# Optimization experiments

Hardware: AMD Instinct MI355X
Metric: run time of the kernel (lower is better)

The kernel has to match this reference:

```python
import jax, jax.numpy as jnp
import numpy as np

N, E = 32768, 524288
NIN = NOUT = 64
EIN = 32
H, C = 4, 64
HC = H * C


def seg_softmax(logits, seg, num):
    m = jax.ops.segment_max(logits, seg, num_segments=num)
    m = jnp.where(jnp.isfinite(m), m, 0.0)
    ex = jnp.exp(logits - m[seg])
    s = jax.ops.segment_sum(ex, seg, num_segments=num)
    return ex / (s[seg] + 1e-16)


def setup_inputs() -> dict:
    key = jax.random.key(0)
    ks = iter(jax.random.split(key, 48))
    rn = lambda shape, s=0.05: jax.random.normal(next(ks), shape, jnp.float32) * s
    z = lambda shape: jnp.zeros(shape, jnp.float32)
    d = dict(
        x=rn((N, NIN), 1.0),
        edge_attr=rn((E, EIN), 1.0),
        # GINEConv 1: nn = mlp1 (64 -> 64 -> 64), edge lin (32 -> 64), eps
        eps1=z(()), w1a=rn((NIN, 64)), b1a=z((64,)), w1b=rn((64, NOUT)), b1b=z((NOUT,)),
        we1=rn((EIN, NIN)), be1=z((NIN,)),
        # GINEConv 2: nn = mlp2 (64 -> 32 -> 64), edge lin (32 -> 64), eps
        eps2=z(()), w2a=rn((NOUT, 32)), b2a=z((32,)), w2b=rn((32, NOUT)), b2b=z((NOUT,)),
        we2=rn((EIN, NOUT)), be2=z((NOUT,)),
        # TransformerConv(64, 64, heads=4, edge_dim=32)
        wq=rn((NOUT, HC)), bq=z((HC,)), wk=rn((NOUT, HC)), bk=z((HC,)),
        wv=rn((NOUT, HC)), bv=z((HC,)), we3=rn((EIN, HC)),
        wskip=rn((NOUT, HC)), bskip=z((HC,)),
        # GATv2Conv(256, 64, heads=1, edge_dim=32)
        wl=rn((HC, NOUT)), bl=z((NOUT,)), wr=rn((HC, NOUT)), br=z((NOUT,)),
        we4=rn((EIN, NOUT)), att=rn((NOUT,)), bias4=z((NOUT,)),
    )
    d['edge_index'] = jax.random.randint(next(ks), (2, E), 0, N, dtype=jnp.int64)
    return d


def _forward(x, edge_attr, eps1, w1a, b1a, w1b, b1b, we1, be1,
             eps2, w2a, b2a, w2b, b2b, we2, be2,
             wq, bq, wk, bk, wv, bv, we3, wskip, bskip,
             wl, bl, wr, br, we4, att, bias4, edge_index):
    src, dst = edge_index[0], edge_index[1]
    n = x.shape[0]

    # --- GINEConv 1: nn((1+eps)*x + sum_j relu(x_j + lin_e(e_ij))) ---
    e1 = edge_attr @ we1 + be1                                  # (E, NIN)
    agg = jax.ops.segment_sum(jax.nn.relu(x[src] + e1), dst, num_segments=n)
    h = (1.0 + eps1) * x + agg
    x = jax.nn.relu(h @ w1a + b1a) @ w1b + b1b                  # (N, NOUT)

    # --- GINEConv 2 ---
    e2 = edge_attr @ we2 + be2
    agg = jax.ops.segment_sum(jax.nn.relu(x[src] + e2), dst, num_segments=n)
    h = (1.0 + eps2) * x + agg
    x = jax.nn.relu(h @ w2a + b2a) @ w2b + b2b                  # (N, NOUT)

    # --- TransformerConv (heads=4, concat, root skip) ---
    q = (x @ wq + bq).reshape(n, H, C)
    k = (x @ wk + bk).reshape(n, H, C)
    v = (x @ wv + bv).reshape(n, H, C)
    e3 = (edge_attr @ we3).reshape(-1, H, C)
    kj = k[src] + e3
    alpha = jnp.einsum('ehc,ehc->eh', q[dst], kj) / jnp.sqrt(jnp.float32(C))
    alpha = seg_softmax(alpha, dst, n)                          # (E, H)
    msg = (v[src] + e3) * alpha[:, :, None]                     # (E, H, C)
    out = jax.ops.segment_sum(msg, dst, num_segments=n).reshape(n, HC)
    x = out + x @ wskip + bskip                                 # (N, 256)

    # --- GATv2Conv (heads=1) ---
    xl = x @ wl + bl                                            # (N, NOUT)
    xr = x @ wr + br
    e4 = edge_attr @ we4
    hmsg = jax.nn.leaky_relu(xl[src] + xr[dst] + e4, 0.2)       # (E, NOUT)
    logit = hmsg @ att                                          # (E,)
    a = seg_softmax(logit, dst, n)
    x = jax.ops.segment_sum(xl[src] * a[:, None], dst, num_segments=n) + bias4
    return x


def reference(x, edge_attr, eps1, w1a, b1a, w1b, b1b, we1, be1,
              eps2, w2a, b2a, w2b, b2b, we2, be2,
              wq, bq, wk, bk, wv, bv, we3, wskip, bskip,
              wl, bl, wr, br, we4, att, bias4, edge_index):
    return _forward(x, edge_attr, eps1, w1a, b1a, w1b, b1b, we1, be1,
                    eps2, w2a, b2a, w2b, b2b, we2, be2,
                    wq, bq, wk, bk, wv, bv, we3, wskip, bskip,
                    wl, bl, wr, br, we4, att, bias4, edge_index)
```

## Files before the change

kernel.cpp:

```cpp
#include <hip/hip_runtime.h>
#include <math.h>


typedef __attribute__((ext_vector_type(2))) _Float16 half2v;
typedef __attribute__((ext_vector_type(4))) _Float16 half4v;
typedef __attribute__((ext_vector_type(8))) _Float16 half8v;
typedef __attribute__((ext_vector_type(4))) float float4v;

__global__ void k_detect(const unsigned int* __restrict__ w, int* __restrict__ flag)
{
    __shared__ int any;
    if (threadIdx.x == 0) any = 0;
    __syncthreads();
    int found = 0;
    for (int i = threadIdx.x; i < 2048; i += 256)
        if (w[2 * i + 1] != 0u) found = 1;
    if (found) atomicOr(&any, 1);
    __syncthreads();
    if (threadIdx.x == 0) flag[0] = any ? 0 : 1;
}

__global__ void k_cvt(const void* __restrict__ eidx, const int* __restrict__ flag,
                      int* __restrict__ out, int* __restrict__ counts, int E)
{
    int i = blockIdx.x * blockDim.x + threadIdx.x;
    if (i >= 2 * E) return;
    int v = flag[0] ? (int)((const long long*)eidx)[i] : ((const int*)eidx)[i];
    out[i] = v;
    if (i >= E) atomicAdd(&counts[v], 1);
}

__global__ void k_scan(const int* __restrict__ counts, int* __restrict__ offs,
                       int* __restrict__ cursor, int N)
{
    __shared__ int part[1024];
    int t = threadIdx.x;
    int base = t * 32;
    int loc[32];
    int s = 0;
#pragma unroll
    for (int i = 0; i < 32; i++) { loc[i] = counts[base + i]; s += loc[i]; }
    part[t] = s;
    __syncthreads();
    for (int off = 1; off < 1024; off <<= 1) {
        int v = (t >= off) ? part[t - off] : 0;
        __syncthreads();
        part[t] += v;
        __syncthreads();
    }
    int run = part[t] - s;
#pragma unroll
    for (int i = 0; i < 32; i++) {
        offs[base + i] = run;
        cursor[base + i] = run;
        run += loc[i];
    }
    if (t == 1023) offs[N] = run;
}

__global__ void k_scatter(const int* __restrict__ dst, const int* __restrict__ srcA,
                          int* __restrict__ cursor, int* __restrict__ perm,
                          int* __restrict__ sperm, int* __restrict__ pos, int E)
{
    int i = blockIdx.x * blockDim.x + threadIdx.x;
    if (i < E) {
        int d = dst[i];
        int p = atomicAdd(&cursor[d], 1);
        perm[p] = i;
        sperm[p] = srcA[i];
        pos[i] = p;
    }
}

__global__ __launch_bounds__(256) void k_eap(const float* __restrict__ ea,
                                             const int* __restrict__ pos,
                                             _Float16* __restrict__ eap)
{
    int t = threadIdx.x;
    int i = blockIdx.x * 64 + (t >> 2);
    int ks = (t & 3) * 8;
    float4 a0 = *(const float4*)&ea[(size_t)i * 32 + ks];
    float4 a1 = *(const float4*)&ea[(size_t)i * 32 + ks + 4];
    half8v h8;
    h8[0] = (_Float16)a0.x; h8[1] = (_Float16)a0.y;
    h8[2] = (_Float16)a0.z; h8[3] = (_Float16)a0.w;
    h8[4] = (_Float16)a1.x; h8[5] = (_Float16)a1.y;
    h8[6] = (_Float16)a1.z; h8[7] = (_Float16)a1.w;
    int p = pos[i];
    *(half8v*)&eap[(size_t)p * 32 + ks] = h8;
}

__global__ __launch_bounds__(256) void k_emm(
    const _Float16* __restrict__ eap,
    const _Float16* __restrict__ WtA, const float* __restrict__ beA,
    _Float16* __restrict__ epA,
    const _Float16* __restrict__ WtB, const float* __restrict__ beB,
    _Float16* __restrict__ epB, int dual)
{
    int t = threadIdx.x;
    int wid = t >> 6, l = t & 63;
    int jb = (blockIdx.x * 4 + wid) * 16;
    int cr = l & 15, kg = l >> 4;
    half8v a = *(const half8v*)&eap[(size_t)(jb + cr) * 32 + kg * 8];
    int orow = kg * 4;
#pragma unroll
    for (int c = 0; c < 4; c++) {
        half8v b = *(const half8v*)&WtA[(size_t)(c * 16 + cr) * 32 + kg * 8];
        float4v d = __builtin_amdgcn_mfma_f32_16x16x32_f16(a, b, (float4v){0.f,0.f,0.f,0.f}, 0, 0, 0);
        int col = c * 16 + cr;
        float bv = beA ? beA[col] : 0.f;
#pragma unroll
        for (int r = 0; r < 4; r++)
            epA[(size_t)(jb + orow + r) * 64 + col] = (_Float16)(d[r] + bv);
    }
    if (dual) {
#pragma unroll
        for (int c = 0; c < 4; c++) {
            half8v b = *(const half8v*)&WtB[(size_t)(c * 16 + cr) * 32 + kg * 8];
            float4v d = __builtin_amdgcn_mfma_f32_16x16x32_f16(a, b, (float4v){0.f,0.f,0.f,0.f}, 0, 0, 0);
            int col = c * 16 + cr;
            float bv = beB ? beB[col] : 0.f;
#pragma unroll
            for (int r = 0; r < 4; r++)
                epB[(size_t)(jb + orow + r) * 64 + col] = (_Float16)(d[r] + bv);
        }
    }
}

__global__ __launch_bounds__(256) void k_egv(
    const float* __restrict__ ea, const int* __restrict__ perm,
    const float* __restrict__ weA, const float* __restrict__ beA,
    _Float16* __restrict__ epA,
    const float* __restrict__ weB, const float* __restrict__ beB,
    _Float16* __restrict__ epB, int dual)
{
    int t = threadIdx.x;
    int wid = t >> 6, lane = t & 63;
    float wA[32];
#pragma unroll
    for (int k = 0; k < 32; k++) wA[k] = weA[k * 64 + lane];
    float bAc = beA ? beA[lane] : 0.f;
    float wB[32];
    float bBc = 0.f;
    if (dual) {
#pragma unroll
        for (int k = 0; k < 32; k++) wB[k] = weB[k * 64 + lane];
        bBc = beB ? beB[lane] : 0.f;
    }
    int jbase = (blockIdx.x * 4 + wid) * 8;
    for (int u = 0; u < 8; u++) {
        int j = jbase + u;
        int e = __builtin_amdgcn_readfirstlane(perm[j]);
        const float4* ea4 = (const float4*)(ea + (size_t)e * 32);
        float eav[32];
#pragma unroll
        for (int w = 0; w < 8; w++) {
            float4 t4 = ea4[w];
            eav[4 * w] = t4.x; eav[4 * w + 1] = t4.y;
            eav[4 * w + 2] = t4.z; eav[4 * w + 3] = t4.w;
        }
        float vA = bAc;
#pragma unroll
        for (int k = 0; k < 32; k++) vA = fmaf(eav[k], wA[k], vA);
        epA[(size_t)j * 64 + lane] = (_Float16)vA;
        if (dual) {
            float vB = bBc;
#pragma unroll
            for (int k = 0; k < 32; k++) vB = fmaf(eav[k], wB[k], vB);
            epB[(size_t)j * 64 + lane] = (_Float16)vB;
        }
    }
}

__global__ __launch_bounds__(256) void k_prep(
    const float* __restrict__ x, int NX,
    const float* __restrict__ wq, const float* __restrict__ wk,
    const float* __restrict__ wv, const float* __restrict__ wskip,
    const float* __restrict__ wl, const float* __restrict__ wr,
    const float* __restrict__ w1a, const float* __restrict__ w1b,
    const float* __restrict__ w2a, const float* __restrict__ w2b,
    const float* __restrict__ we3, const float* __restrict__ bq,
    const float* __restrict__ we1, const float* __restrict__ we2,
    const float* __restrict__ we4,
    _Float16* __restrict__ xh,
    _Float16* __restrict__ Wtq, _Float16* __restrict__ Wtk,
    _Float16* __restrict__ Wtv, _Float16* __restrict__ Wts,
    _Float16* __restrict__ Wtl, _Float16* __restrict__ Wtr,
    _Float16* __restrict__ Wt1a, _Float16* __restrict__ Wt1b,
    _Float16* __restrict__ Wt2a, _Float16* __restrict__ Wt2b,
    _Float16* __restrict__ Mt, float* __restrict__ cst,
    _Float16* __restrict__ we3r,
    _Float16* __restrict__ Wt1e, _Float16* __restrict__ Wt2e,
    _Float16* __restrict__ Wt4e)
{
    int g = blockIdx.x * 256 + threadIdx.x;
    if (g < 16384) {
        int c = g >> 6, k = g & 63;
        Wtq[g] = (_Float16)wq[(size_t)k * 256 + c];
        Wtk[g] = (_Float16)wk[(size_t)k * 256 + c];
        Wtv[g] = (_Float16)wv[(size_t)k * 256 + c];
        Wts[g] = (_Float16)wskip[(size_t)k * 256 + c];
    } else if (g < 32768) {
        int q = g - 16384, c = q >> 8, k = q & 255;
        Wtl[q] = (_Float16)wl[(size_t)k * 64 + c];
        Wtr[q] = (_Float16)wr[(size_t)k * 64 + c];
    } else if (g < 36864) {
        int q = g - 32768, m = q >> 6, k = q & 63;
        Wt1a[q] = (_Float16)w1a[(size_t)k * 64 + m];
        Wt1b[q] = (_Float16)w1b[(size_t)k * 64 + m];
    } else if (g < 38912) {
        int q = g - 36864, m = q >> 6, k = q & 63;
        Wt2a[q] = (_Float16)w2a[(size_t)k * 32 + m];
    } else if (g < 40960) {
        int q = g - 38912, c = q >> 5, k = q & 31;
        Wt2b[q] = (_Float16)w2b[(size_t)k * 64 + c];
    } else if (g < 49152) {
        int q = g - 40960, m = q >> 6, d = q & 63;
        int h = m >> 5, kk = m & 31;
        float s = 0.f;
        for (int c = 0; c < 64; c++)
            s = fmaf(wq[(size_t)d * 256 + h * 64 + c],
                     we3[(size_t)kk * 256 + h * 64 + c], s);
        Mt[q] = (_Float16)(0.125f * s);
    } else if (g < 49280) {
        int m = g - 49152, h = m >> 5, kk = m & 31;
        float s = 0.f;
        for (int c = 0; c < 64; c++)
            s = fmaf(bq[h * 64 + c], we3[(size_t)kk * 256 + h * 64 + c], s);
        cst[m] = 0.125f * s;
    } else if (g < 57472) {
        int q = g - 49280;
        int kk = q >> 10, ph = (q >> 9) & 1, lane = (q >> 3) & 63, i = q & 7;
        int slot = lane >> 4, hh = (lane >> 2) & 3, ss = lane & 3;
        we3r[q] = (_Float16)we3[(size_t)(slot * 8 + kk) * 256
                                + hh * 64 + ss * 16 + ph * 8 + i];
    } else if (g < 59520) {
        int q = g - 57472, c = q >> 5, k = q & 31;
        Wt1e[q] = (_Float16)we1[(size_t)k * 64 + c];
    } else if (g < 61568) {
        int q = g - 59520, c = q >> 5, k = q & 31;
        Wt2e[q] = (_Float16)we2[(size_t)k * 64 + c];
    } else if (g < 63616) {
        int q = g - 61568, c = q >> 5, k = q & 31;
        Wt4e[q] = (_Float16)we4[(size_t)k * 64 + c];
    }
    for (int i = g; i < NX; i += 256 * 256)
        xh[i] = (_Float16)x[i];
}

template<int MID>
__global__ __launch_bounds__(256) void k_mlp(
    const _Float16* __restrict__ A,
    const _Float16* __restrict__ Wt1, const float* __restrict__ b1,
    const _Float16* __restrict__ Wt2, const float* __restrict__ b2,
    _Float16* __restrict__ out)
{
    __shared__ _Float16 As[64][72];
    __shared__ _Float16 Ws1[MID][72];
    __shared__ _Float16 Ws2[64][MID + 8];
    __shared__ _Float16 mids[64][MID + 8];
    int t = threadIdx.x;
    int n0 = blockIdx.x * 64;
    for (int f = t; f < 512; f += 256) {
        int r = f >> 3, seg = f & 7;
        *(uint4*)&As[r][seg * 8] = *(const uint4*)&A[(size_t)(n0 + r) * 64 + seg * 8];
    }
    for (int f = t; f < MID * 8; f += 256) {
        int r = f >> 3, seg = f & 7;
        *(uint4*)&Ws1[r][seg * 8] = *(const uint4*)&Wt1[(size_t)r * 64 + seg * 8];
    }
    constexpr int CH = MID / 8;
    for (int f = t; f < 64 * CH; f += 256) {
        int r = f / CH, seg = f % CH;
        *(uint4*)&Ws2[r][seg * 8] = *(const uint4*)&Wt2[(size_t)r * MID + seg * 8];
    }
    __syncthreads();
    int w = t >> 6, l = t & 63;
    int arow = w * 16 + (l & 15);
    int kg = (l >> 4) * 8;
    int colg = l & 15;
    int orow = w * 16 + (l >> 4) * 4;
    half8v a0 = *(const half8v*)&As[arow][kg];
    half8v a1 = *(const half8v*)&As[arow][32 + kg];
    constexpr int NCT1 = MID / 16;
#pragma unroll
    for (int ct = 0; ct < NCT1; ct++) {
        half8v b0 = *(const half8v*)&Ws1[ct * 16 + colg][kg];
        half8v b1v = *(const half8v*)&Ws1[ct * 16 + colg][32 + kg];
        float4v acc = {0.f, 0.f, 0.f, 0.f};
        acc = __builtin_amdgcn_mfma_f32_16x16x32_f16(a0, b0, acc, 0, 0, 0);
        acc = __builtin_amdgcn_mfma_f32_16x16x32_f16(a1, b1v, acc, 0, 0, 0);
        int col = ct * 16 + colg;
        float bb = b1[col];
#pragma unroll
        for (int r = 0; r < 4; r++)
            mids[orow + r][col] = (_Float16)fmaxf(acc[r] + bb, 0.f);
    }
    __syncthreads();
    half8v m0 = *(const half8v*)&mids[arow][kg];
#pragma unroll
    for (int ct = 0; ct < 4; ct++) {
        half8v b0 = *(const half8v*)&Ws2[ct * 16 + colg][kg];
        float4v acc = {0.f, 0.f, 0.f, 0.f};
        acc = __builtin_amdgcn_mfma_f32_16x16x32_f16(m0, b0, acc, 0, 0, 0);
        if (MID == 64) {
            half8v m1 = *(const half8v*)&mids[arow][32 + kg];
            half8v b1v = *(const half8v*)&Ws2[ct * 16 + colg][32 + kg];
            acc = __builtin_amdgcn_mfma_f32_16x16x32_f16(m1, b1v, acc, 0, 0, 0);
        }
        int col = ct * 16 + colg;
        float bb = b2[col];
#pragma unroll
        for (int r = 0; r < 4; r++)
            out[(size_t)(n0 + orow + r) * 64 + col] = (_Float16)(acc[r] + bb);
    }
}

__global__ __launch_bounds__(256) void k_gemm4m(
    const _Float16* __restrict__ A,
    const _Float16* __restrict__ Wtq, const float* __restrict__ bq,
    const _Float16* __restrict__ Wtk, const float* __restrict__ bk,
    const _Float16* __restrict__ Wtv, const float* __restrict__ bv,
    const _Float16* __restrict__ Wts, const float* __restrict__ bs,
    const _Float16* __restrict__ Mt,  const float* __restrict__ cst,
    _Float16* __restrict__ qbh, _Float16* __restrict__ kbh,
    _Float16* __restrict__ vbh, float* __restrict__ skipb,
    _Float16* __restrict__ qtp)
{
    __shared__ _Float16 As[64][72];
    __shared__ _Float16 Ws[128][72];
    int t = threadIdx.x;
    int n0 = blockIdx.x * 64;
    int y = blockIdx.y;
    for (int f = t; f < 512; f += 256) {
        int r = f >> 3, seg = f & 7;
        *(uint4*)&As[r][seg * 8] = *(const uint4*)&A[(size_t)(n0 + r) * 64 + seg * 8];
    }
    if (y < 16) {
        int p = y >> 2, j0 = (y & 3) * 64;
        const _Float16* Wt = (p == 0) ? Wtq : (p == 1) ? Wtk : (p == 2) ? Wtv : Wts;
        for (int f = t; f < 512; f += 256) {
            int c = f >> 3, seg = f & 7;
            *(uint4*)&Ws[c][seg * 8] = *(const uint4*)&Wt[(size_t)(j0 + c) * 64 + seg * 8];
        }
    } else {
        for (int f = t; f < 1024; f += 256) {
            int c = f >> 3, seg = f & 7;
            *(uint4*)&Ws[c][seg * 8] = *(const uint4*)&Mt[(size_t)c * 64 + seg * 8];
        }
    }
    __syncthreads();
    int w = t >> 6, l = t & 63;
    int arow = w * 16 + (l & 15);
    int kg = (l >> 4) * 8;
    int colg = l & 15;
    int orow = w * 16 + (l >> 4) * 4;
    half8v a0 = *(const half8v*)&As[arow][kg];
    half8v a1 = *(const half8v*)&As[arow][32 + kg];
    if (y < 16) {
        int p = y >> 2, j0 = (y & 3) * 64;
        const float* B = (p == 0) ? bq : (p == 1) ? bk : (p == 2) ? bv : bs;
        float4v acc[4];
#pragma unroll
        for (int ct = 0; ct < 4; ct++) {
            half8v b0 = *(const half8v*)&Ws[ct * 16 + colg][kg];
            half8v b1 = *(const half8v*)&Ws[ct * 16 + colg][32 + kg];
            float4v a = {0.f, 0.f, 0.f, 0.f};
            a = __builtin_amdgcn_mfma_f32_16x16x32_f16(a0, b0, a, 0, 0, 0);
            a = __builtin_amdgcn_mfma_f32_16x16x32_f16(a1, b1, a, 0, 0, 0);
            acc[ct] = a;
        }
#pragma unroll
        for (int ct = 0; ct < 4; ct++) {
            int col = j0 + ct * 16 + colg;
            float bb = B[col];
            if (p == 3) {
#pragma unroll
                for (int r = 0; r < 4; r++)
                    skipb[(size_t)(n0 + orow + r) * 256 + col] = acc[ct][r] + bb;
            } else {
                _Float16* O = (p == 0) ? qbh : (p == 1) ? kbh : vbh;
#pragma unroll
                for (int r = 0; r < 4; r++)
                    O[(size_t)(n0 + orow + r) * 256 + col] = (_Float16)(acc[ct][r] + bb);
            }
        }
    } else {
        float4v acc[8];
#pragma unroll
        for (int ct = 0; ct < 8; ct++) {
            half8v b0 = *(const half8v*)&Ws[ct * 16 + colg][kg];
            half8v b1 = *(const half8v*)&Ws[ct * 16 + colg][32 + kg];
            float4v a = {0.f, 0.f, 0.f, 0.f};
            a = __builtin_amdgcn_mfma_f32_16x16x32_f16(a0, b0, a, 0, 0, 0);
            a = __builtin_amdgcn_mfma_f32_16x16x32_f16(a1, b1, a, 0, 0, 0);
            acc[ct] = a;
        }
#pragma unroll
        for (int ct = 0; ct < 8; ct++) {
            int col = ct * 16 + colg;
            float bb = cst[col];
#pragma unroll
            for (int r = 0; r < 4; r++)
                qtp[(size_t)(n0 + orow + r) * 128 + col] = (_Float16)(acc[ct][r] + bb);
        }
    }
}

__global__ __launch_bounds__(256) void k_gatgemm(
    const float* __restrict__ A,
    const _Float16* __restrict__ WtL, const float* __restrict__ bL,
    const _Float16* __restrict__ WtR, const float* __restrict__ bR,
    _Float16* __restrict__ xlh, _Float16* __restrict__ xrh)
{
    __shared__ _Float16 As[64][136];
    __shared__ _Float16 Ws[64][136];
    int t = threadIdx.x;
    int n0 = blockIdx.x * 64;
    int y = blockIdx.y;
    const _Float16* Wt = y ? WtR : WtL;
    const float* bb = y ? bR : bL;
    _Float16* out = y ? xrh : xlh;
    int w = t >> 6, l = t & 63;
    int arow = w * 16 + (l & 15);
    int kg = (l >> 4) * 8;
    int colg = l & 15;
    int orow = w * 16 + (l >> 4) * 4;
    float4v acc[4] = {{0.f,0.f,0.f,0.f},{0.f,0.f,0.f,0.f},
                      {0.f,0.f,0.f,0.f},{0.f,0.f,0.f,0.f}};
    for (int kh = 0; kh < 2; kh++) {
        __syncthreads();
        for (int f = t; f < 2048; f += 256) {
            int r = f >> 5, seg = f & 31;
            float4 v = *(const float4*)&A[(size_t)(n0 + r) * 256 + kh * 128 + seg * 4];
            half4v hv;
            hv[0] = (_Float16)v.x; hv[1] = (_Float16)v.y;
            hv[2] = (_Float16)v.z; hv[3] = (_Float16)v.w;
            *(half4v*)&As[r][seg * 4] = hv;
        }
        for (int f = t; f < 1024; f += 256) {
            int c = f >> 4, seg = f & 15;
            *(uint4*)&Ws[c][seg * 8] = *(const uint4*)&Wt[(size_t)c * 256 + kh * 128 + seg * 8];
        }
        __syncthreads();
#pragma unroll
        for (int ks = 0; ks < 4; ks++) {
            half8v a = *(const half8v*)&As[arow][ks * 32 + kg];
#pragma unroll
            for (int ct = 0; ct < 4; ct++) {
                half8v b = *(const half8v*)&Ws[ct * 16 + colg][ks * 32 + kg];
                acc[ct] = __builtin_amdgcn_mfma_f32_16x16x32_f16(a, b, acc[ct], 0, 0, 0);
            }
        }
    }
#pragma unroll
    for (int ct = 0; ct < 4; ct++) {
        int col = ct * 16 + colg;
        float bv = bb[col];
#pragma unroll
        for (int r = 0; r < 4; r++)
            out[(size_t)(n0 + orow + r) * 64 + col] = (_Float16)(acc[ct][r] + bv);
    }
}

__global__ __launch_bounds__(256) void k_gine2(
    const _Float16* __restrict__ xin, const _Float16* __restrict__ ep,
    const float* __restrict__ epsp,
    const int* __restrict__ offs, const int* __restrict__ sperm,
    _Float16* __restrict__ hout)
{
    int t = threadIdx.x;
    int wid  = __builtin_amdgcn_readfirstlane(t >> 6);
    int n    = blockIdx.x * 4 + wid;
    int lane = t & 63;
    int g = lane >> 4, li = lane & 15, c0 = li * 4;
    int j0 = __builtin_amdgcn_readfirstlane(offs[n]);
    int j1 = __builtin_amdgcn_readfirstlane(offs[n + 1]);
    float4 acc = {0.f, 0.f, 0.f, 0.f};
    for (int jq = j0; jq < j1; jq += 4) {
        int j = jq + g;
        int jc = (j < j1) ? j : (j1 - 1);
        int s = sperm[jc];
        half4v ev = *(const half4v*)&ep[(size_t)jc * 64 + c0];
        half4v xv = *(const half4v*)&xin[(size_t)s * 64 + c0];
        if (j < j1) {
            acc.x += fmaxf((float)xv[0] + (float)ev[0], 0.f);
            acc.y += fmaxf((float)xv[1] + (float)ev[1], 0.f);
            acc.z += fmaxf((float)xv[2] + (float)ev[2], 0.f);
            acc.w += fmaxf((float)xv[3] + (float)ev[3], 0.f);
        }
    }
    acc.x += __shfl_xor(acc.x, 16); acc.x += __shfl_xor(acc.x, 32);
    acc.y += __shfl_xor(acc.y, 16); acc.y += __shfl_xor(acc.y, 32);
    acc.z += __shfl_xor(acc.z, 16); acc.z += __shfl_xor(acc.z, 32);
    acc.w += __shfl_xor(acc.w, 16); acc.w += __shfl_xor(acc.w, 32);
    if (g == 0) {
        float eps1 = 1.f + epsp[0];
        half4v xn = *(const half4v*)&xin[(size_t)n * 64 + c0];
        half4v o;
        o[0] = (_Float16)(eps1 * (float)xn[0] + acc.x);
        o[1] = (_Float16)(eps1 * (float)xn[1] + acc.y);
        o[2] = (_Float16)(eps1 * (float)xn[2] + acc.z);
        o[3] = (_Float16)(eps1 * (float)xn[3] + acc.w);
        *(half4v*)&hout[(size_t)n * 64 + c0] = o;
    }
}

template<int USE_EAP>
__global__ __launch_bounds__(256) void k_tconv4(
    const _Float16* __restrict__ qb, const _Float16* __restrict__ kb,
    const _Float16* __restrict__ vb, const _Float16* __restrict__ qtp,
    const _Float16* __restrict__ we3r, const _Float16* __restrict__ eap,
    const float* __restrict__ ea, const int* __restrict__ perm,
    const int* __restrict__ offs, const int* __restrict__ sperm,
    float* __restrict__ skip_io)
{
    __shared__ _Float16 we3s[8192];
    __shared__ float wa_s[4][4][32];
    int t = threadIdx.x;
    ((uint4*)we3s)[t]       = ((const uint4*)we3r)[t];
    ((uint4*)we3s)[t + 256] = ((const uint4*)we3r)[t + 256];
    ((uint4*)we3s)[t + 512] = ((const uint4*)we3r)[t + 512];
    ((uint4*)we3s)[t + 768] = ((const uint4*)we3r)[t + 768];
    int wid = __builtin_amdgcn_readfirstlane(t >> 6);
    int n = blockIdx.x * 4 + wid;
    int lane = t & 63;
    int g = lane >> 4, li = lane & 15;
    int h = li >> 2, sub = li & 3;
    int ch0 = h * 64 + sub * 16;
    float qs[16];
    {
        half8v q0 = *(const half8v*)&qb[(size_t)n * 256 + ch0];
        half8v q1 = *(const half8v*)&qb[(size_t)n * 256 + ch0 + 8];
#pragma unroll
        for (int i = 0; i < 8; i++) {
            qs[i] = (float)q0[i] * 0.125f;
            qs[8 + i] = (float)q1[i] * 0.125f;
        }
    }
    float qtf[8];
    {
        half8v qt8 = *(const half8v*)&qtp[(size_t)n * 128 + h * 32 + sub * 8];
#pragma unroll
        for (int i = 0; i < 8; i++) qtf[i] = (float)qt8[i];
    }
    int j0 = __builtin_amdgcn_readfirstlane(offs[n]);
    int j1 = __builtin_amdgcn_readfirstlane(offs[n + 1]);
    float l = 0.f;
    float acc[16] = {};
    float wa[8] = {};
    for (int jq = j0; jq < j1; jq += 4) {
        int j = jq + g;
        int jc = (j < j1) ? j : (j1 - 1);
        int s = sperm[jc];
        const _Float16* kr = &kb[(size_t)s * 256 + ch0];
        half8v k0 = *(const half8v*)kr;
        half8v k1 = *(const half8v*)(kr + 8);
        float ef[8];
        if (USE_EAP) {
            half8v e8 = *(const half8v*)&eap[(size_t)jc * 32 + sub * 8];
#pragma unroll
            for (int i = 0; i < 8; i++) ef[i] = (float)e8[i];
        } else {
            int e = perm[jc];
            float4 a0 = *(const float4*)&ea[(size_t)e * 32 + sub * 8];
            float4 a1 = *(const float4*)&ea[(size_t)e * 32 + sub * 8 + 4];
            ef[0] = a0.x; ef[1] = a0.y; ef[2] = a0.z; ef[3] = a0.w;
            ef[4] = a1.x; ef[5] = a1.y; ef[6] = a1.z; ef[7] = a1.w;
        }
        float p = 0.f;
#pragma unroll
        for (int i = 0; i < 8; i++)
            p += qs[i] * (float)k0[i] + qs[8 + i] * (float)k1[i];
#pragma unroll
        for (int i = 0; i < 8; i++) p += qtf[i] * ef[i];
        p += __shfl_xor(p, 1);
        p += __shfl_xor(p, 2);
        float w = (j < j1) ? __expf(p) : 0.f;
        const _Float16* vr = &vb[(size_t)s * 256 + ch0];
        half8v v0 = *(const half8v*)vr;
        half8v v1 = *(const half8v*)(vr + 8);
        l += w;
#pragma unroll
        for (int i = 0; i < 8; i++) {
            acc[i] = fmaf(w, (float)v0[i], acc[i]);
            acc[8 + i] = fmaf(w, (float)v1[i], acc[8 + i]);
        }
#pragma unroll
        for (int i = 0; i < 8; i++) wa[i] = fmaf(w, ef[i], wa[i]);
    }
    l += __shfl_xor(l, 16); l += __shfl_xor(l, 32);
#pragma unroll
    for (int i = 0; i < 16; i++) {
        acc[i] += __shfl_xor(acc[i], 16);
        acc[i] += __shfl_xor(acc[i], 32);
    }
#pragma unroll
    for (int i = 0; i < 8; i++) {
        wa[i] += __shfl_xor(wa[i], 16);
        wa[i] += __shfl_xor(wa[i], 32);
    }
    if (g == 0) {
#pragma unroll
        for (int i = 0; i < 8; i++) wa_s[wid][h][sub * 8 + i] = wa[i];
    }
    __syncthreads();
    float corr[16] = {};
#pragma unroll
    for (int kk = 0; kk < 8; kk++) {
        float wv = wa_s[wid][h][g * 8 + kk];
        half8v w3a = *(const half8v*)&we3s[kk * 1024 + lane * 8];
        half8v w3b = *(const half8v*)&we3s[kk * 1024 + 512 + lane * 8];
#pragma unroll
        for (int i = 0; i < 8; i++) {
            corr[i] = fmaf(wv, (float)w3a[i], corr[i]);
            corr[8 + i] = fmaf(wv, (float)w3b[i], corr[8 + i]);
        }
    }
#pragma unroll
    for (int i = 0; i < 16; i++) {
        corr[i] += __shfl_xor(corr[i], 16);
        corr[i] += __shfl_xor(corr[i], 32);
    }
    if (g == 0) {
        float rl = 1.f / (l + 1e-16f);
        size_t o = (size_t)n * 256 + ch0;
#pragma unroll
        for (int i = 0; i < 16; i += 4) {
            float4 sk = *(const float4*)&skip_io[o + i];
            float4 ov;
            ov.x = (acc[i]     + corr[i])     * rl + sk.x;
            ov.y = (acc[i + 1] + corr[i + 1]) * rl + sk.y;
            ov.z = (acc[i + 2] + corr[i + 2]) * rl + sk.z;
            ov.w = (acc[i + 3] + corr[i + 3]) * rl + sk.w;
            *(float4*)&skip_io[o + i] = ov;
        }
    }
}

__global__ __launch_bounds__(256) void k_gat2(
    const _Float16* __restrict__ xl, const _Float16* __restrict__ xr,
    const _Float16* __restrict__ e4p,
    const float* __restrict__ attv, const float* __restrict__ bias4,
    const int* __restrict__ offs, const int* __restrict__ sperm,
    float* __restrict__ out)
{
    int t = threadIdx.x;
    int wid  = __builtin_amdgcn_readfirstlane(t >> 6);
    int n    = blockIdx.x * 4 + wid;
    int lane = t & 63;
    int g = lane >> 4, li = lane & 15, c0 = li * 4;
    half4v xrh = *(const half4v*)&xr[(size_t)n * 64 + c0];
    float xr0 = (float)xrh[0], xr1 = (float)xrh[1];
    float xr2 = (float)xrh[2], xr3 = (float)xrh[3];
    float4 av  = *(const float4*)&attv[c0];
    int j0 = __builtin_amdgcn_readfirstlane(offs[n]);
    int j1 = __builtin_amdgcn_readfirstlane(offs[n + 1]);
    float l = 0.f;
    float4 acc = {0.f, 0.f, 0.f, 0.f};
    for (int jq = j0; jq < j1; jq += 4) {
        int j = jq + g;
        int jc = (j < j1) ? j : (j1 - 1);
        int s = sperm[jc];
        half4v ev = *(const half4v*)&e4p[(size_t)jc * 64 + c0];
        half4v xlv = *(const half4v*)&xl[(size_t)s * 64 + c0];
        float x0 = (float)xlv[0], x1 = (float)xlv[1];
        float x2 = (float)xlv[2], x3 = (float)xlv[3];
        float h0 = x0 + xr0 + (float)ev[0];
        float h1 = x1 + xr1 + (float)ev[1];
        float h2 = x2 + xr2 + (float)ev[2];
        float h3 = x3 + xr3 + (float)ev[3];
        h0 = (h0 > 0.f) ? h0 : 0.2f * h0;
        h1 = (h1 > 0.f) ? h1 : 0.2f * h1;
        h2 = (h2 > 0.f) ? h2 : 0.2f * h2;
        h3 = (h3 > 0.f) ? h3 : 0.2f * h3;
        float p = h0 * av.x + h1 * av.y + h2 * av.z + h3 * av.w;
        p += __shfl_xor(p, 1); p += __shfl_xor(p, 2);
        p += __shfl_xor(p, 4); p += __shfl_xor(p, 8);
        float w = (j < j1) ? __expf(p) : 0.f;
        l += w;
        acc.x = fmaf(w, x0, acc.x);
        acc.y = fmaf(w, x1, acc.y);
        acc.z = fmaf(w, x2, acc.z);
        acc.w = fmaf(w, x3, acc.w);
    }
    l += __shfl_xor(l, 16); l += __shfl_xor(l, 32);
    acc.x += __shfl_xor(acc.x, 16); acc.x += __shfl_xor(acc.x, 32);
    acc.y += __shfl_xor(acc.y, 16); acc.y += __shfl_xor(acc.y, 32);
    acc.z += __shfl_xor(acc.z, 16); acc.z += __shfl_xor(acc.z, 32);
    acc.w += __shfl_xor(acc.w, 16); acc.w += __shfl_xor(acc.w, 32);
    if (g == 0) {
        float rl = 1.f / (l + 1e-16f);
        float4 bv = *(const float4*)&bias4[c0];
        float4 o;
        o.x = acc.x * rl + bv.x;
        o.y = acc.y * rl + bv.y;
        o.z = acc.z * rl + bv.z;
        o.w = acc.w * rl + bv.w;
        *(float4*)&out[(size_t)n * 64 + c0] = o;
    }
}

extern "C" void kernel_launch(void* const* d_in, const int* in_sizes, int n_in,
                              void* d_out, int out_size, void* d_ws, size_t ws_size,
                              hipStream_t stream)
{
    const float* x     = (const float*)d_in[0];
    const float* ea    = (const float*)d_in[1];
    const float* eps1  = (const float*)d_in[2];
    const float* w1a   = (const float*)d_in[3];
    const float* b1a   = (const float*)d_in[4];
    const float* w1b   = (const float*)d_in[5];
    const float* b1b   = (const float*)d_in[6];
    const float* we1   = (const float*)d_in[7];
    const float* be1   = (const float*)d_in[8];
    const float* eps2  = (const float*)d_in[9];
    const float* w2a   = (const float*)d_in[10];
    const float* b2a   = (const float*)d_in[11];
    const float* w2b   = (const float*)d_in[12];
    const float* b2b   = (const float*)d_in[13];
    const float* we2   = (const float*)d_in[14];
    const float* be2   = (const float*)d_in[15];
    const float* wq    = (const float*)d_in[16];
    const float* bq    = (const float*)d_in[17];
    const float* wk    = (const float*)d_in[18];
    const float* bk    = (const float*)d_in[19];
    const float* wv    = (const float*)d_in[20];
    const float* bv    = (const float*)d_in[21];
    const float* we3   = (const float*)d_in[22];
    const float* wskip = (const float*)d_in[23];
    const float* bskip = (const float*)d_in[24];
    const float* wl    = (const float*)d_in[25];
    const float* bl    = (const float*)d_in[26];
    const float* wr    = (const float*)d_in[27];
    const float* br    = (const float*)d_in[28];
    const float* we4   = (const float*)d_in[29];
    const float* attv  = (const float*)d_in[30];
    const float* bias4 = (const float*)d_in[31];
    const void*  eidx  = d_in[32];

    const int N = in_sizes[0] / 64;
    const int E = in_sizes[1] / 32;

    char* ws = (char*)d_ws;
    size_t off = 0;
    auto alloc = [&](size_t bytes) {
        void* p = ws + off;
        off += (bytes + 255) & ~(size_t)255;
        return p;
    };
    int* flag    = (int*)alloc(4);
    int* econv   = (int*)alloc((size_t)2 * E * 4);
    int* counts  = (int*)alloc((size_t)N * 4);
    int* cursor  = (int*)alloc((size_t)N * 4);
    int* offs    = (int*)alloc((size_t)(N + 1) * 4);
    int* perm    = (int*)alloc((size_t)E * 4);
    int* sperm   = (int*)alloc((size_t)E * 4);
    int* pos     = (int*)alloc((size_t)E * 4);
    _Float16* xh  = (_Float16*)alloc((size_t)N * 64 * 2);
    _Float16* h16 = (_Float16*)alloc((size_t)N * 64 * 2);
    _Float16* x1h = (_Float16*)alloc((size_t)N * 64 * 2);
    _Float16* x2h = (_Float16*)alloc((size_t)N * 64 * 2);
    _Float16* Wtq = (_Float16*)alloc(16384 * 2);
    _Float16* Wtk = (_Float16*)alloc(16384 * 2);
    _Float16* Wtv = (_Float16*)alloc(16384 * 2);
    _Float16* Wts = (_Float16*)alloc(16384 * 2);
    _Float16* Wtl = (_Float16*)alloc(16384 * 2);
    _Float16* Wtr = (_Float16*)alloc(16384 * 2);
    _Float16* Wt1a = (_Float16*)alloc(4096 * 2);
    _Float16* Wt1b = (_Float16*)alloc(4096 * 2);
    _Float16* Wt2a = (_Float16*)alloc(2048 * 2);
    _Float16* Wt2b = (_Float16*)alloc(2048 * 2);
    _Float16* Mt   = (_Float16*)alloc(8192 * 2);
    float*    cst  = (float*)alloc(128 * 4);
    _Float16* we3r = (_Float16*)alloc(8192 * 2);
    _Float16* Wt1e = (_Float16*)alloc(2048 * 2);
    _Float16* Wt2e = (_Float16*)alloc(2048 * 2);
    _Float16* Wt4e = (_Float16*)alloc(2048 * 2);
    char* R = (char*)alloc((size_t)2 * E * 64 * 2);
    _Float16* e1p   = (_Float16*)R;
    _Float16* e2p   = e1p + (size_t)E * 64;
    _Float16* qbh   = (_Float16*)R;
    _Float16* kbh   = qbh + (size_t)N * 256;
    _Float16* vbh   = kbh + (size_t)N * 256;
    float*    skipb = (float*)(R + (size_t)3 * N * 256 * 2);
    _Float16* qtp   = (_Float16*)(R + (size_t)3 * N * 256 * 2 + (size_t)N * 256 * 4);
    _Float16* e4p   = (_Float16*)R;
    _Float16* xlh   = h16;
    _Float16* xrh   = x1h;
    size_t base_off = off;
    _Float16* eap = (_Float16*)alloc((size_t)E * 32 * 2);
    int use_eap = (off <= ws_size) ? 1 : 0;

    if (base_off > ws_size) return;

    k_prep<<<256, 256, 0, stream>>>(x, N * 64, wq, wk, wv, wskip, wl, wr,
                                    w1a, w1b, w2a, w2b, we3, bq, we1, we2, we4,
                                    xh, Wtq, Wtk, Wtv, Wts, Wtl, Wtr,
                                    Wt1a, Wt1b, Wt2a, Wt2b, Mt, cst,
                                    we3r, Wt1e, Wt2e, Wt4e);

    k_detect<<<1, 256, 0, stream>>>((const unsigned int*)eidx, flag);
    hipMemsetAsync(counts, 0, (size_t)N * 4, stream);
    k_cvt<<<(2 * E + 255) / 256, 256, 0, stream>>>(eidx, flag, econv, counts, E);
    const int* srcI = econv;
    const int* dstI = econv + E;

    k_scan<<<1, 1024, 0, stream>>>(counts, offs, cursor, N);
    k_scatter<<<(E + 255) / 256, 256, 0, stream>>>(dstI, srcI, cursor, perm, sperm,
                                                   pos, E);

    if (use_eap) {
        k_eap<<<E / 64, 256, 0, stream>>>(ea, pos, eap);
        k_emm<<<E / 64, 256, 0, stream>>>(eap, Wt1e, be1, e1p, Wt2e, be2, e2p, 1);
    } else {
        k_egv<<<E / 32, 256, 0, stream>>>(ea, perm, we1, be1, e1p, we2, be2, e2p, 1);
    }

    k_gine2<<<N / 4, 256, 0, stream>>>(xh, e1p, eps1, offs, sperm, h16);
    k_mlp<64><<<N / 64, 256, 0, stream>>>(h16, Wt1a, b1a, Wt1b, b1b, x1h);

    k_gine2<<<N / 4, 256, 0, stream>>>(x1h, e2p, eps2, offs, sperm, h16);
    k_mlp<32><<<N / 64, 256, 0, stream>>>(h16, Wt2a, b2a, Wt2b, b2b, x2h);

    k_gemm4m<<<dim3(N / 64, 17), 256, 0, stream>>>(x2h,
                                                   Wtq, bq, Wtk, bk, Wtv, bv,
                                                   Wts, bskip, Mt, cst,
                                                   qbh, kbh, vbh, skipb, qtp);
    if (use_eap)
        k_tconv4<1><<<N / 4, 256, 0, stream>>>(qbh, kbh, vbh, qtp, we3r, eap,
                                               ea, perm, offs, sperm, skipb);
    else
        k_tconv4<0><<<N / 4, 256, 0, stream>>>(qbh, kbh, vbh, qtp, we3r, eap,
                                               ea, perm, offs, sperm, skipb);

    k_gatgemm<<<dim3(N / 64, 2), 256, 0, stream>>>(skipb, Wtl, bl, Wtr, br, xlh, xrh);
    if (use_eap)
        k_emm<<<E / 64, 256, 0, stream>>>(eap, Wt4e, (const float*)nullptr, e4p,
                                          (const _Float16*)nullptr,
                                          (const float*)nullptr,
                                          (_Float16*)nullptr, 0);
    else
        k_egv<<<E / 32, 256, 0, stream>>>(ea, perm, we4, (const float*)nullptr, e4p,
                                          (const float*)nullptr,
                                          (const float*)nullptr,
                                          (_Float16*)nullptr, 0);
    k_gat2<<<N / 4, 256, 0, stream>>>(xlh, xrh, e4p, attv, bias4, offs, sperm,
                                      (float*)d_out);
}
```

Before: 401.4 us.

## Fold Q/K/V projections into 64-dim source features for transformer conv

Rewrites the TransformerConv stage algebraically. Attention logits now come from a precomputed Wq·Wk^T product applied to the destination node, dotted with the raw 64-dim source features. Values are aggregated in input space and projected once per node by a new post kernel, using a concatenated [Wv; We3] matrix. This removes the per-node K/V 256-wide GEMM outputs and shrinks per-edge gather traffic. It also fuses the edge-attr fp16 permutation into the scatter kernel and merges the two GAT linear GEMMs into one launch. The costs are an extra kernel and fp16 intermediate buffers, which may change numerical precision.

```diff
diff --git a/kernel.cpp b/kernel.cpp
--- a/kernel.cpp
+++ b/kernel.cpp
@@ -58,36 +58,32 @@
     if (t == 1023) offs[N] = run;
 }
 
+template<int WEAP>
 __global__ void k_scatter(const int* __restrict__ dst, const int* __restrict__ srcA,
                           int* __restrict__ cursor, int* __restrict__ perm,
-                          int* __restrict__ sperm, int* __restrict__ pos, int E)
+                          int* __restrict__ sperm, const float* __restrict__ ea,
+                          _Float16* __restrict__ eap, int E)
 {
     int i = blockIdx.x * blockDim.x + threadIdx.x;
-    if (i < E) {
-        int d = dst[i];
-        int p = atomicAdd(&cursor[d], 1);
-        perm[p] = i;
-        sperm[p] = srcA[i];
-        pos[i] = p;
-    }
-}
-
-__global__ __launch_bounds__(256) void k_eap(const float* __restrict__ ea,
-                                             const int* __restrict__ pos,
-                                             _Float16* __restrict__ eap)
-{
-    int t = threadIdx.x;
-    int i = blockIdx.x * 64 + (t >> 2);
-    int ks = (t & 3) * 8;
-    float4 a0 = *(const float4*)&ea[(size_t)i * 32 + ks];
-    float4 a1 = *(const float4*)&ea[(size_t)i * 32 + ks + 4];
-    half8v h8;
-    h8[0] = (_Float16)a0.x; h8[1] = (_Float16)a0.y;
-    h8[2] = (_Float16)a0.z; h8[3] = (_Float16)a0.w;
-    h8[4] = (_Float16)a1.x; h8[5] = (_Float16)a1.y;
-    h8[6] = (_Float16)a1.z; h8[7] = (_Float16)a1.w;
-    int p = pos[i];
-    *(half8v*)&eap[(size_t)p * 32 + ks] = h8;
+    if (i >= E) return;
+    int d = dst[i];
+    int p = atomicAdd(&cursor[d], 1);
+    perm[p] = i;
+    sperm[p] = srcA[i];
+    if (WEAP) {
+        const float4* r = (const float4*)(ea + (size_t)i * 32);
+        half8v* o = (half8v*)(eap + (size_t)p * 32);
+#pragma unroll
+        for (int w = 0; w < 4; w++) {
+            float4 a = r[2 * w], b = r[2 * w + 1];
+            half8v h8;
+            h8[0] = (_Float16)a.x; h8[1] = (_Float16)a.y;
+            h8[2] = (_Float16)a.z; h8[3] = (_Float16)a.w;
+            h8[4] = (_Float16)b.x; h8[5] = (_Float16)b.y;
+            h8[6] = (_Float16)b.z; h8[7] = (_Float16)b.w;
+            o[w] = h8;
+        }
+    }
 }
 
 __global__ __launch_bounds__(256) void k_emm(
@@ -183,68 +179,79 @@
     const float* __restrict__ we1, const float* __restrict__ we2,
     const float* __restrict__ we4,
     _Float16* __restrict__ xh,
-    _Float16* __restrict__ Wtq, _Float16* __restrict__ Wtk,
-    _Float16* __restrict__ Wtv, _Float16* __restrict__ Wts,
+    _Float16* __restrict__ Wts, _Float16* __restrict__ Gt,
     _Float16* __restrict__ Wtl, _Float16* __restrict__ Wtr,
     _Float16* __restrict__ Wt1a, _Float16* __restrict__ Wt1b,
     _Float16* __restrict__ Wt2a, _Float16* __restrict__ Wt2b,
     _Float16* __restrict__ Mt, float* __restrict__ cst,
-    _Float16* __restrict__ we3r,
     _Float16* __restrict__ Wt1e, _Float16* __restrict__ Wt2e,
-    _Float16* __restrict__ Wt4e)
+    _Float16* __restrict__ Wt4e, float* __restrict__ zt,
+    _Float16* __restrict__ Bt3)
 {
     int g = blockIdx.x * 256 + threadIdx.x;
     if (g < 16384) {
         int c = g >> 6, k = g & 63;
-        Wtq[g] = (_Float16)wq[(size_t)k * 256 + c];
-        Wtk[g] = (_Float16)wk[(size_t)k * 256 + c];
-        Wtv[g] = (_Float16)wv[(size_t)k * 256 + c];
         Wts[g] = (_Float16)wskip[(size_t)k * 256 + c];
     } else if (g < 32768) {
-        int q = g - 16384, c = q >> 8, k = q & 255;
+        int q = g - 16384, col = q >> 6, d = q & 63;
+        int h = col >> 6, c = col & 63;
+        float s = 0.f;
+        for (int mq = 0; mq < 64; mq++)
+            s = fmaf(wq[(size_t)d * 256 + h * 64 + mq],
+                     wk[(size_t)c * 256 + h * 64 + mq], s);
+        Gt[q] = (_Float16)(0.125f * s);
+    } else if (g < 49152) {
+        int q = g - 32768, c = q >> 8, k = q & 255;
         Wtl[q] = (_Float16)wl[(size_t)k * 64 + c];
         Wtr[q] = (_Float16)wr[(size_t)k * 64 + c];
-    } else if (g < 36864) {
-        int q = g - 32768, m = q >> 6, k = q & 63;
+    } else if (g < 53248) {
+        int q = g - 49152, m = q >> 6, k = q & 63;
         Wt1a[q] = (_Float16)w1a[(size_t)k * 64 + m];
         Wt1b[q] = (_Float16)w1b[(size_t)k * 64 + m];
-    } else if (g < 38912) {
-        int q = g - 36864, m = q >> 6, k = q & 63;
+    } else if (g < 55296) {
+        int q = g - 53248, m = q >> 6, k = q & 63;
         Wt2a[q] = (_Float16)w2a[(size_t)k * 32 + m];
-    } else if (g < 40960) {
-        int q = g - 38912, c = q >> 5, k = q & 31;
+    } else if (g < 57344) {
+        int q = g - 55296, c = q >> 5, k = q & 31;
         Wt2b[q] = (_Float16)w2b[(size_t)k * 64 + c];
-    } else if (g < 49152) {
-        int q = g - 40960, m = q >> 6, d = q & 63;
+    } else if (g < 65536) {
+        int q = g - 57344, m = q >> 6, d = q & 63;
         int h = m >> 5, kk = m & 31;
         float s = 0.f;
         for (int c = 0; c < 64; c++)
             s = fmaf(wq[(size_t)d * 256 + h * 64 + c],
                      we3[(size_t)kk * 256 + h * 64 + c], s);
         Mt[q] = (_Float16)(0.125f * s);
-    } else if (g < 49280) {
-        int m = g - 49152, h = m >> 5, kk = m & 31;
+    } else if (g < 65664) {
+        int m = g - 65536, h = m >> 5, kk = m & 31;
         float s = 0.f;
         for (int c = 0; c < 64; c++)
             s = fmaf(bq[h * 64 + c], we3[(size_t)kk * 256 + h * 64 + c], s);
         cst[m] = 0.125f * s;
-    } else if (g < 57472) {
-        int q = g - 49280;
-        int kk = q >> 10, ph = (q >> 9) & 1, lane = (q >> 3) & 63, i = q & 7;
-        int slot = lane >> 4, hh = (lane >> 2) & 3, ss = lane & 3;
-        we3r[q] = (_Float16)we3[(size_t)(slot * 8 + kk) * 256
-                                + hh * 64 + ss * 16 + ph * 8 + i];
-    } else if (g < 59520) {
-        int q = g - 57472, c = q >> 5, k = q & 31;
+    } else if (g < 67712) {
+        int q = g - 65664, c = q >> 5, k = q & 31;
         Wt1e[q] = (_Float16)we1[(size_t)k * 64 + c];
-    } else if (g < 61568) {
-        int q = g - 59520, c = q >> 5, k = q & 31;
+    } else if (g < 69760) {
+        int q = g - 67712, c = q >> 5, k = q & 31;
         Wt2e[q] = (_Float16)we2[(size_t)k * 64 + c];
-    } else if (g < 63616) {
-        int q = g - 61568, c = q >> 5, k = q & 31;
+    } else if (g < 71808) {
+        int q = g - 69760, c = q >> 5, k = q & 31;
         Wt4e[q] = (_Float16)we4[(size_t)k * 64 + c];
-    }
-    for (int i = g; i < NX; i += 256 * 256)
+    } else if (g < 72064) {
+        int q = g - 71808, h = q >> 6, c = q & 63;
+        float s = 0.f;
+        for (int mq = 0; mq < 64; mq++)
+            s = fmaf(wk[(size_t)c * 256 + h * 64 + mq], bq[h * 64 + mq], s);
+        zt[q] = 0.125f * s;
+    } else if (g < 96640) {
+        int q = g - 72064;
+        int hc = q / 96, k = q - hc * 96;
+        int h = hc >> 6, col = hc & 63;
+        float v = (k < 64) ? wv[(size_t)k * 256 + h * 64 + col]
+                           : we3[(size_t)(k - 64) * 256 + h * 64 + col];
+        Bt3[q] = (_Float16)v;
+    }
+    for (int i = g; i < NX; i += 512 * 256)
         xh[i] = (_Float16)x[i];
 }
 
@@ -318,13 +325,10 @@
 
 __global__ __launch_bounds__(256) void k_gemm4m(
     const _Float16* __restrict__ A,
-    const _Float16* __restrict__ Wtq, const float* __restrict__ bq,
-    const _Float16* __restrict__ Wtk, const float* __restrict__ bk,
-    const _Float16* __restrict__ Wtv, const float* __restrict__ bv,
+    const _Float16* __restrict__ Gt,
     const _Float16* __restrict__ Wts, const float* __restrict__ bs,
     const _Float16* __restrict__ Mt,  const float* __restrict__ cst,
-    _Float16* __restrict__ qbh, _Float16* __restrict__ kbh,
-    _Float16* __restrict__ vbh, float* __restrict__ skipb,
+    _Float16* __restrict__ Yb, _Float16* __restrict__ skiph,
     _Float16* __restrict__ qtp)
 {
     __shared__ _Float16 As[64][72];
@@ -336,9 +340,9 @@
         int r = f >> 3, seg = f & 7;
         *(uint4*)&As[r][seg * 8] = *(const uint4*)&A[(size_t)(n0 + r) * 64 + seg * 8];
     }
-    if (y < 16) {
-        int p = y >> 2, j0 = (y & 3) * 64;
-        const _Float16* Wt = (p == 0) ? Wtq : (p == 1) ? Wtk : (p == 2) ? Wtv : Wts;
+    if (y < 8) {
+        int j0 = (y & 3) * 64;
+        const _Float16* Wt = (y < 4) ? Gt : Wts;
         for (int f = t; f < 512; f += 256) {
             int c = f >> 3, seg = f & 7;
             *(uint4*)&Ws[c][seg * 8] = *(const uint4*)&Wt[(size_t)(j0 + c) * 64 + seg * 8];
@@ -357,10 +361,9 @@
     int orow = w * 16 + (l >> 4) * 4;
     half8v a0 = *(const half8v*)&As[arow][kg];
     half8v a1 = *(const half8v*)&As[arow][32 + kg];
-    if (y < 16) {
-        int p = y >> 2, j0 = (y & 3) * 64;
-        const float* B = (p == 0) ? bq : (p == 1) ? bk : (p == 2) ? bv : bs;
-        float4v acc[4];
+    if (y < 8) {
+        int j0 = (y & 3) * 64;
+        _Float16* O = (y < 4) ? Yb : skiph;
 #pragma unroll
         for (int ct = 0; ct < 4; ct++) {
             half8v b0 = *(const half8v*)&Ws[ct * 16 + colg][kg];
@@ -368,25 +371,13 @@
             float4v a = {0.f, 0.f, 0.f, 0.f};
             a = __builtin_amdgcn_mfma_f32_16x16x32_f16(a0, b0, a, 0, 0, 0);
             a = __builtin_amdgcn_mfma_f32_16x16x32_f16(a1, b1, a, 0, 0, 0);
-            acc[ct] = a;
-        }
-#pragma unroll
-        for (int ct = 0; ct < 4; ct++) {
             int col = j0 + ct * 16 + colg;
-            float bb = B[col];
-            if (p == 3) {
-#pragma unroll
-                for (int r = 0; r < 4; r++)
-                    skipb[(size_t)(n0 + orow + r) * 256 + col] = acc[ct][r] + bb;
-            } else {
-                _Float16* O = (p == 0) ? qbh : (p == 1) ? kbh : vbh;
-#pragma unroll
-                for (int r = 0; r < 4; r++)
-                    O[(size_t)(n0 + orow + r) * 256 + col] = (_Float16)(acc[ct][r] + bb);
-            }
+            float bb = (y < 4) ? 0.f : bs[col];
+#pragma unroll
+            for (int r = 0; r < 4; r++)
+                O[(size_t)(n0 + orow + r) * 256 + col] = (_Float16)(a[r] + bb);
         }
     } else {
-        float4v acc[8];
 #pragma unroll
         for (int ct = 0; ct < 8; ct++) {
             half8v b0 = *(const half8v*)&Ws[ct * 16 + colg][kg];
@@ -394,72 +385,12 @@
             float4v a = {0.f, 0.f, 0.f, 0.f};
             a = __builtin_amdgcn_mfma_f32_16x16x32_f16(a0, b0, a, 0, 0, 0);
             a = __builtin_amdgcn_mfma_f32_16x16x32_f16(a1, b1, a, 0, 0, 0);
-            acc[ct] = a;
-        }
-#pragma unroll
-        for (int ct = 0; ct < 8; ct++) {
             int col = ct * 16 + colg;
             float bb = cst[col];
 #pragma unroll
             for (int r = 0; r < 4; r++)
-                qtp[(size_t)(n0 + orow + r) * 128 + col] = (_Float16)(acc[ct][r] + bb);
-        }
-    }
-}
-
-__global__ __launch_bounds__(256) void k_gatgemm(
-    const float* __restrict__ A,
-    const _Float16* __restrict__ WtL, const float* __restrict__ bL,
-    const _Float16* __restrict__ WtR, const float* __restrict__ bR,
-    _Float16* __restrict__ xlh, _Float16* __restrict__ xrh)
-{
-    __shared__ _Float16 As[64][136];
-    __shared__ _Float16 Ws[64][136];
-    int t = threadIdx.x;
-    int n0 = blockIdx.x * 64;
-    int y = blockIdx.y;
-    const _Float16* Wt = y ? WtR : WtL;
-    const float* bb = y ? bR : bL;
-    _Float16* out = y ? xrh : xlh;
-    int w = t >> 6, l = t & 63;
-    int arow = w * 16 + (l & 15);
-    int kg = (l >> 4) * 8;
-    int colg = l & 15;
-    int orow = w * 16 + (l >> 4) * 4;
-    float4v acc[4] = {{0.f,0.f,0.f,0.f},{0.f,0.f,0.f,0.f},
-                      {0.f,0.f,0.f,0.f},{0.f,0.f,0.f,0.f}};
-    for (int kh = 0; kh < 2; kh++) {
-        __syncthreads();
-        for (int f = t; f < 2048; f += 256) {
-            int r = f >> 5, seg = f & 31;
-            float4 v = *(const float4*)&A[(size_t)(n0 + r) * 256 + kh * 128 + seg * 4];
-            half4v hv;
-            hv[0] = (_Float16)v.x; hv[1] = (_Float16)v.y;
-            hv[2] = (_Float16)v.z; hv[3] = (_Float16)v.w;
-            *(half4v*)&As[r][seg * 4] = hv;
-        }
-        for (int f = t; f < 1024; f += 256) {
-            int c = f >> 4, seg = f & 15;
-            *(uint4*)&Ws[c][seg * 8] = *(const uint4*)&Wt[(size_t)c * 256 + kh * 128 + seg * 8];
-        }
-        __syncthreads();
-#pragma unroll
-        for (int ks = 0; ks < 4; ks++) {
-            half8v a = *(const half8v*)&As[arow][ks * 32 + kg];
-#pragma unroll
-            for (int ct = 0; ct < 4; ct++) {
-                half8v b = *(const half8v*)&Ws[ct * 16 + colg][ks * 32 + kg];
-                acc[ct] = __builtin_amdgcn_mfma_f32_16x16x32_f16(a, b, acc[ct], 0, 0, 0);
-            }
-        }
-    }
-#pragma unroll
-    for (int ct = 0; ct < 4; ct++) {
-        int col = ct * 16 + colg;
-        float bv = bb[col];
-#pragma unroll
-        for (int r = 0; r < 4; r++)
-            out[(size_t)(n0 + orow + r) * 64 + col] = (_Float16)(acc[ct][r] + bv);
+                qtp[(size_t)(n0 + orow + r) * 128 + col] = (_Float16)(a[r] + bb);
+        }
     }
 }
 
@@ -507,133 +438,205 @@
 }
 
 template<int USE_EAP>
-__global__ __launch_bounds__(256) void k_tconv4(
-    const _Float16* __restrict__ qb, const _Float16* __restrict__ kb,
-    const _Float16* __restrict__ vb, const _Float16* __restrict__ qtp,
-    const _Float16* __restrict__ we3r, const _Float16* __restrict__ eap,
-    const float* __restrict__ ea, const int* __restrict__ perm,
-    const int* __restrict__ offs, const int* __restrict__ sperm,
-    float* __restrict__ skip_io)
-{
-    __shared__ _Float16 we3s[8192];
-    __shared__ float wa_s[4][4][32];
-    int t = threadIdx.x;
-    ((uint4*)we3s)[t]       = ((const uint4*)we3r)[t];
-    ((uint4*)we3s)[t + 256] = ((const uint4*)we3r)[t + 256];
-    ((uint4*)we3s)[t + 512] = ((const uint4*)we3r)[t + 512];
-    ((uint4*)we3s)[t + 768] = ((const uint4*)we3r)[t + 768];
+__global__ __launch_bounds__(256) void k_tconv5(
+    const _Float16* __restrict__ Yb, const _Float16* __restrict__ qtp,
+    const float* __restrict__ zt, const _Float16* __restrict__ x2h,
+    const _Float16* __restrict__ eap, const float* __restrict__ ea,
+    const int* __restrict__ perm, const int* __restrict__ offs,
+    const int* __restrict__ sperm,
+    _Float16* __restrict__ xaccb, _Float16* __restrict__ wab,
+    float* __restrict__ lb)
+{
+    int t = threadIdx.x;
     int wid = __builtin_amdgcn_readfirstlane(t >> 6);
     int n = blockIdx.x * 4 + wid;
     int lane = t & 63;
-    int g = lane >> 4, li = lane & 15;
-    int h = li >> 2, sub = li & 3;
-    int ch0 = h * 64 + sub * 16;
-    float qs[16];
+    int h = lane >> 4, c = lane & 15;
+    float yb0, yb1, yb2, yb3;
     {
-        half8v q0 = *(const half8v*)&qb[(size_t)n * 256 + ch0];
-        half8v q1 = *(const half8v*)&qb[(size_t)n * 256 + ch0 + 8];
-#pragma unroll
-        for (int i = 0; i < 8; i++) {
-            qs[i] = (float)q0[i] * 0.125f;
-            qs[8 + i] = (float)q1[i] * 0.125f;
-        }
-    }
-    float qtf[8];
-    {
-        half8v qt8 = *(const half8v*)&qtp[(size_t)n * 128 + h * 32 + sub * 8];
-#pragma unroll
-        for (int i = 0; i < 8; i++) qtf[i] = (float)qt8[i];
-    }
+        half4v Y4 = *(const half4v*)&Yb[(size_t)n * 256 + h * 64 + c * 4];
+        float4 z4 = *(const float4*)&zt[h * 64 + c * 4];
+        yb0 = (float)Y4[0] + z4.x; yb1 = (float)Y4[1] + z4.y;
+        yb2 = (float)Y4[2] + z4.z; yb3 = (float)Y4[3] + z4.w;
+    }
+    half2v qt2 = *(const half2v*)&qtp[(size_t)n * 128 + h * 32 + c * 2];
+    float qt0 = (float)qt2[0], qt1 = (float)qt2[1];
     int j0 = __builtin_amdgcn_readfirstlane(offs[n]);
     int j1 = __builtin_amdgcn_readfirstlane(offs[n + 1]);
     float l = 0.f;
-    float acc[16] = {};
-    float wa[8] = {};
-    for (int jq = j0; jq < j1; jq += 4) {
-        int j = jq + g;
-        int jc = (j < j1) ? j : (j1 - 1);
-        int s = sperm[jc];
-        const _Float16* kr = &kb[(size_t)s * 256 + ch0];
-        half8v k0 = *(const half8v*)kr;
-        half8v k1 = *(const half8v*)(kr + 8);
-        float ef[8];
+    float xa0 = 0.f, xa1 = 0.f, xa2 = 0.f, xa3 = 0.f;
+    float wa0 = 0.f, wa1 = 0.f;
+    int j = j0;
+    for (; j + 1 < j1; j += 2) {
+        int s0 = __builtin_amdgcn_readfirstlane(sperm[j]);
+        int s1 = __builtin_amdgcn_readfirstlane(sperm[j + 1]);
+        half4v xA = *(const half4v*)&x2h[(size_t)s0 * 64 + c * 4];
+        half4v xB = *(const half4v*)&x2h[(size_t)s1 * 64 + c * 4];
+        float eA0, eA1, eB0, eB1;
         if (USE_EAP) {
-            half8v e8 = *(const half8v*)&eap[(size_t)jc * 32 + sub * 8];
-#pragma unroll
-            for (int i = 0; i < 8; i++) ef[i] = (float)e8[i];
+            half2v vA = *(const half2v*)&eap[(size_t)j * 32 + c * 2];
+            half2v vB = *(const half2v*)&eap[(size_t)(j + 1) * 32 + c * 2];
+            eA0 = (float)vA[0]; eA1 = (float)vA[1];
+            eB0 = (float)vB[0]; eB1 = (float)vB[1];
         } else {
-            int e = perm[jc];
-            float4 a0 = *(const float4*)&ea[(size_t)e * 32 + sub * 8];
-            float4 a1 = *(const float4*)&ea[(size_t)e * 32 + sub * 8 + 4];
-            ef[0] = a0.x; ef[1] = a0.y; ef[2] = a0.z; ef[3] = a0.w;
-            ef[4] = a1.x; ef[5] = a1.y; ef[6] = a1.z; ef[7] = a1.w;
-        }
-        float p = 0.f;
-#pragma unroll
-        for (int i = 0; i < 8; i++)
-            p += qs[i] * (float)k0[i] + qs[8 + i] * (float)k1[i];
-#pragma unroll
-        for (int i = 0; i < 8; i++) p += qtf[i] * ef[i];
-        p += __shfl_xor(p, 1);
-        p += __shfl_xor(p, 2);
-        float w = (j < j1) ? __expf(p) : 0.f;
-        const _Float16* vr = &vb[(size_t)s * 256 + ch0];
-        half8v v0 = *(const half8v*)vr;
-        half8v v1 = *(const half8v*)(vr + 8);
-        l += w;
-#pragma unroll
-        for (int i = 0; i < 8; i++) {
-            acc[i] = fmaf(w, (float)v0[i], acc[i]);
-            acc[8 + i] = fmaf(w, (float)v1[i], acc[8 + i]);
-        }
-#pragma unroll
-        for (int i = 0; i < 8; i++) wa[i] = fmaf(w, ef[i], wa[i]);
-    }
-    l += __shfl_xor(l, 16); l += __shfl_xor(l, 32);
-#pragma unroll
-    for (int i = 0; i < 16; i++) {
-        acc[i] += __shfl_xor(acc[i], 16);
-        acc[i] += __shfl_xor(acc[i], 32);
-    }
-#pragma unroll
-    for (int i = 0; i < 8; i++) {
-        wa[i] += __shfl_xor(wa[i], 16);
-        wa[i] += __shfl_xor(wa[i], 32);
-    }
-    if (g == 0) {
-#pragma unroll
-        for (int i = 0; i < 8; i++) wa_s[wid][h][sub * 8 + i] = wa[i];
-    }
-    __syncthreads();
-    float corr[16] = {};
-#pragma unroll
-    for (int kk = 0; kk < 8; kk++) {
-        float wv = wa_s[wid][h][g * 8 + kk];
-        half8v w3a = *(const half8v*)&we3s[kk * 1024 + lane * 8];
-        half8v w3b = *(const half8v*)&we3s[kk * 1024 + 512 + lane * 8];
-#pragma unroll
-        for (int i = 0; i < 8; i++) {
-            corr[i] = fmaf(wv, (float)w3a[i], corr[i]);
-            corr[8 + i] = fmaf(wv, (float)w3b[i], corr[8 + i]);
-        }
-    }
-#pragma unroll
-    for (int i = 0; i < 16; i++) {
-        corr[i] += __shfl_xor(corr[i], 16);
-        corr[i] += __shfl_xor(corr[i], 32);
-    }
-    if (g == 0) {
-        float rl = 1.f / (l + 1e-16f);
-        size_t o = (size_t)n * 256 + ch0;
-#pragma unroll
-        for (int i = 0; i < 16; i += 4) {
-            float4 sk = *(const float4*)&skip_io[o + i];
-            float4 ov;
-            ov.x = (acc[i]     + corr[i])     * rl + sk.x;
-            ov.y = (acc[i + 1] + corr[i + 1]) * rl + sk.y;
-            ov.z = (acc[i + 2] + corr[i + 2]) * rl + sk.z;
-            ov.w = (acc[i + 3] + corr[i + 3]) * rl + sk.w;
-            *(float4*)&skip_io[o + i] = ov;
+            int e0 = __builtin_amdgcn_readfirstlane(perm[j]);
+            int e1 = __builtin_amdgcn_readfirstlane(perm[j + 1]);
+            float2 fA = *(const float2*)&ea[(size_t)e0 * 32 + c * 2];
+            float2 fB = *(const float2*)&ea[(size_t)e1 * 32 + c * 2];
+            eA0 = fA.x; eA1 = fA.y; eB0 = fB.x; eB1 = fB.y;
+        }
+        float xA0 = (float)xA[0], xA1f = (float)xA[1];
+        float xA2 = (float)xA[2], xA3 = (float)xA[3];
+        float xB0 = (float)xB[0], xB1f = (float)xB[1];
+        float xB2 = (float)xB[2], xB3 = (float)xB[3];
+        float p0 = yb0 * xA0 + yb1 * xA1f + yb2 * xA2 + yb3 * xA3
+                 + qt0 * eA0 + qt1 * eA1;
+        float p1 = yb0 * xB0 + yb1 * xB1f + yb2 * xB2 + yb3 * xB3
+                 + qt0 * eB0 + qt1 * eB1;
+        p0 += __shfl_xor(p0, 1); p1 += __shfl_xor(p1, 1);
+        p0 += __shfl_xor(p0, 2); p1 += __shfl_xor(p1, 2);
+        p0 += __shfl_xor(p0, 4); p1 += __shfl_xor(p1, 4);
+        p0 += __shfl_xor(p0, 8); p1 += __shfl_xor(p1, 8);
+        float w0 = __expf(p0), w1 = __expf(p1);
+        l += w0 + w1;
+        xa0 += w0 * xA0 + w1 * xB0;
+        xa1 += w0 * xA1f + w1 * xB1f;
+        xa2 += w0 * xA2 + w1 * xB2;
+        xa3 += w0 * xA3 + w1 * xB3;
+        wa0 += w0 * eA0 + w1 * eB0;
+        wa1 += w0 * eA1 + w1 * eB1;
+    }
+    if (j < j1) {
+        int s0 = __builtin_amdgcn_readfirstlane(sperm[j]);
+        half4v xA = *(const half4v*)&x2h[(size_t)s0 * 64 + c * 4];
+        float eA0, eA1;
+        if (USE_EAP) {
+            half2v vA = *(const half2v*)&eap[(size_t)j * 32 + c * 2];
+            eA0 = (float)vA[0]; eA1 = (float)vA[1];
+        } else {
+            int e0 = __builtin_amdgcn_readfirstlane(perm[j]);
+            float2 fA = *(const float2*)&ea[(size_t)e0 * 32 + c * 2];
+            eA0 = fA.x; eA1 = fA.y;
+        }
+        float xA0 = (float)xA[0], xA1f = (float)xA[1];
+        float xA2 = (float)xA[2], xA3 = (float)xA[3];
+        float p0 = yb0 * xA0 + yb1 * xA1f + yb2 * xA2 + yb3 * xA3
+                 + qt0 * eA0 + qt1 * eA1;
+        p0 += __shfl_xor(p0, 1); p0 += __shfl_xor(p0, 2);
+        p0 += __shfl_xor(p0, 4); p0 += __shfl_xor(p0, 8);
+        float w0 = __expf(p0);
+        l += w0;
+        xa0 += w0 * xA0; xa1 += w0 * xA1f; xa2 += w0 * xA2; xa3 += w0 * xA3;
+        wa0 += w0 * eA0; wa1 += w0 * eA1;
+    }
+    half4v xo;
+    xo[0] = (_Float16)xa0; xo[1] = (_Float16)xa1;
+    xo[2] = (_Float16)xa2; xo[3] = (_Float16)xa3;
+    *(half4v*)&xaccb[(size_t)n * 256 + h * 64 + c * 4] = xo;
+    half2v wo;
+    wo[0] = (_Float16)wa0; wo[1] = (_Float16)wa1;
+    *(half2v*)&wab[(size_t)n * 128 + h * 32 + c * 2] = wo;
+    if (c == 0) lb[n * 4 + h] = l;
+}
+
+__global__ __launch_bounds__(256) void k_tpost(
+    const _Float16* __restrict__ xaccb, const _Float16* __restrict__ wab,
+    const float* __restrict__ lb, const _Float16* __restrict__ Bt3,
+    const float* __restrict__ bv, _Float16* __restrict__ skiph)
+{
+    int t = threadIdx.x;
+    int h = t >> 6;
+    int l = t & 63;
+    int n0 = blockIdx.x * 64;
+    int colg = l & 15, kg = (l >> 4) * 8;
+    half8v Bf[4][3];
+#pragma unroll
+    for (int ct = 0; ct < 4; ct++) {
+        size_t cb = (size_t)(h * 64 + ct * 16 + colg) * 96;
+        Bf[ct][0] = *(const half8v*)&Bt3[cb + kg];
+        Bf[ct][1] = *(const half8v*)&Bt3[cb + 32 + kg];
+        Bf[ct][2] = *(const half8v*)&Bt3[cb + 64 + kg];
+    }
+#pragma unroll
+    for (int rt = 0; rt < 4; rt++) {
+        int arow = n0 + rt * 16 + (l & 15);
+        half8v A0 = *(const half8v*)&xaccb[(size_t)arow * 256 + h * 64 + kg];
+        half8v A1 = *(const half8v*)&xaccb[(size_t)arow * 256 + h * 64 + 32 + kg];
+        half8v A2 = *(const half8v*)&wab[(size_t)arow * 128 + h * 32 + kg];
+#pragma unroll
+        for (int ct = 0; ct < 4; ct++) {
+            float4v acc = {0.f, 0.f, 0.f, 0.f};
+            acc = __builtin_amdgcn_mfma_f32_16x16x32_f16(A0, Bf[ct][0], acc, 0, 0, 0);
+            acc = __builtin_amdgcn_mfma_f32_16x16x32_f16(A1, Bf[ct][1], acc, 0, 0, 0);
+            acc = __builtin_amdgcn_mfma_f32_16x16x32_f16(A2, Bf[ct][2], acc, 0, 0, 0);
+            int col = h * 64 + ct * 16 + colg;
+            float bvc = bv[col];
+#pragma unroll
+            for (int r = 0; r < 4; r++) {
+                int row = n0 + rt * 16 + (l >> 4) * 4 + r;
+                float lv = lb[row * 4 + h];
+                float rl = (lv > 0.f) ? 1.f / lv : 0.f;
+                float bterm = (lv > 0.f) ? bvc : 0.f;
+                size_t o = (size_t)row * 256 + col;
+                float out = acc[r] * rl + bterm + (float)skiph[o];
+                skiph[o] = (_Float16)out;
+            }
+        }
+    }
+}
+
+__global__ __launch_bounds__(256) void k_gatgemm(
+    const _Float16* __restrict__ A,
+    const _Float16* __restrict__ WtL, const float* __restrict__ bL,
+    const _Float16* __restrict__ WtR, const float* __restrict__ bR,
+    _Float16* __restrict__ xlh, _Float16* __restrict__ xrh)
+{
+    __shared__ _Float16 As[64][136];
+    __shared__ _Float16 WsL[64][136];
+    __shared__ _Float16 WsR[64][136];
+    int t = threadIdx.x;
+    int n0 = blockIdx.x * 64;
+    int w = t >> 6, l = t & 63;
+    int arow = w * 16 + (l & 15);
+    int kg = (l >> 4) * 8;
+    int colg = l & 15;
+    int orow = w * 16 + (l >> 4) * 4;
+    float4v accL[4] = {{0.f,0.f,0.f,0.f},{0.f,0.f,0.f,0.f},
+                       {0.f,0.f,0.f,0.f},{0.f,0.f,0.f,0.f}};
+    float4v accR[4] = {{0.f,0.f,0.f,0.f},{0.f,0.f,0.f,0.f},
+                       {0.f,0.f,0.f,0.f},{0.f,0.f,0.f,0.f}};
+    for (int kh = 0; kh < 2; kh++) {
+        __syncthreads();
+        for (int f = t; f < 1024; f += 256) {
+            int r = f >> 4, seg = f & 15;
+            *(uint4*)&As[r][seg * 8] =
+                *(const uint4*)&A[(size_t)(n0 + r) * 256 + kh * 128 + seg * 8];
+            *(uint4*)&WsL[r][seg * 8] =
+                *(const uint4*)&WtL[(size_t)r * 256 + kh * 128 + seg * 8];
+            *(uint4*)&WsR[r][seg * 8] =
+                *(const uint4*)&WtR[(size_t)r * 256 + kh * 128 + seg * 8];
+        }
+        __syncthreads();
+#pragma unroll
+        for (int ks = 0; ks < 4; ks++) {
+            half8v a = *(const half8v*)&As[arow][ks * 32 + kg];
+#pragma unroll
+            for (int ct = 0; ct < 4; ct++) {
+                half8v bl_ = *(const half8v*)&WsL[ct * 16 + colg][ks * 32 + kg];
+                half8v br_ = *(const half8v*)&WsR[ct * 16 + colg][ks * 32 + kg];
+                accL[ct] = __builtin_amdgcn_mfma_f32_16x16x32_f16(a, bl_, accL[ct], 0, 0, 0);
+                accR[ct] = __builtin_amdgcn_mfma_f32_16x16x32_f16(a, br_, accR[ct], 0, 0, 0);
+            }
+        }
+    }
+#pragma unroll
+    for (int ct = 0; ct < 4; ct++) {
+        int col = ct * 16 + colg;
+        float bvL = bL[col], bvR = bR[col];
+#pragma unroll
+        for (int r = 0; r < 4; r++) {
+            xlh[(size_t)(n0 + orow + r) * 64 + col] = (_Float16)(accL[ct][r] + bvL);
+            xrh[(size_t)(n0 + orow + r) * 64 + col] = (_Float16)(accR[ct][r] + bvR);
         }
     }
 }
@@ -726,7 +729,7 @@
     const float* wk    = (const float*)d_in[18];
     const float* bk    = (const float*)d_in[19];
     const float* wv    = (const float*)d_in[20];
-    const float* bv    = (const float*)d_in[21];
+    const float* bvv   = (const float*)d_in[21];
     const float* we3   = (const float*)d_in[22];
     const float* wskip = (const float*)d_in[23];
     const float* bskip = (const float*)d_in[24];
@@ -738,6 +741,7 @@
     const float* attv  = (const float*)d_in[30];
     const float* bias4 = (const float*)d_in[31];
     const void*  eidx  = d_in[32];
+    (void)bk;
 
     const int N = in_sizes[0] / 64;
     const int E = in_sizes[1] / 32;
@@ -756,49 +760,48 @@
     int* offs    = (int*)alloc((size_t)(N + 1) * 4);
     int* perm    = (int*)alloc((size_t)E * 4);
     int* sperm   = (int*)alloc((size_t)E * 4);
-    int* pos     = (int*)alloc((size_t)E * 4);
     _Float16* xh  = (_Float16*)alloc((size_t)N * 64 * 2);
     _Float16* h16 = (_Float16*)alloc((size_t)N * 64 * 2);
     _Float16* x1h = (_Float16*)alloc((size_t)N * 64 * 2);
     _Float16* x2h = (_Float16*)alloc((size_t)N * 64 * 2);
-    _Float16* Wtq = (_Float16*)alloc(16384 * 2);
-    _Float16* Wtk = (_Float16*)alloc(16384 * 2);
-    _Float16* Wtv = (_Float16*)alloc(16384 * 2);
-    _Float16* Wts = (_Float16*)alloc(16384 * 2);
-    _Float16* Wtl = (_Float16*)alloc(16384 * 2);
-    _Float16* Wtr = (_Float16*)alloc(16384 * 2);
+    _Float16* Wts  = (_Float16*)alloc(16384 * 2);
+    _Float16* Gt   = (_Float16*)alloc(16384 * 2);
+    _Float16* Wtl  = (_Float16*)alloc(16384 * 2);
+    _Float16* Wtr  = (_Float16*)alloc(16384 * 2);
     _Float16* Wt1a = (_Float16*)alloc(4096 * 2);
     _Float16* Wt1b = (_Float16*)alloc(4096 * 2);
     _Float16* Wt2a = (_Float16*)alloc(2048 * 2);
     _Float16* Wt2b = (_Float16*)alloc(2048 * 2);
     _Float16* Mt   = (_Float16*)alloc(8192 * 2);
     float*    cst  = (float*)alloc(128 * 4);
-    _Float16* we3r = (_Float16*)alloc(8192 * 2);
     _Float16* Wt1e = (_Float16*)alloc(2048 * 2);
     _Float16* Wt2e = (_Float16*)alloc(2048 * 2);
     _Float16* Wt4e = (_Float16*)alloc(2048 * 2);
+    float*    zt   = (float*)alloc(256 * 4);
+    _Float16* Bt3  = (_Float16*)alloc(24576 * 2);
     char* R = (char*)alloc((size_t)2 * E * 64 * 2);
-    _Float16* e1p   = (_Float16*)R;
-    _Float16* e2p   = e1p + (size_t)E * 64;
-    _Float16* qbh   = (_Float16*)R;
-    _Float16* kbh   = qbh + (size_t)N * 256;
-    _Float16* vbh   = kbh + (size_t)N * 256;
-    float*    skipb = (float*)(R + (size_t)3 * N * 256 * 2);
-    _Float16* qtp   = (_Float16*)(R + (size_t)3 * N * 256 * 2 + (size_t)N * 256 * 4);
-    _Float16* e4p   = (_Float16*)R;
-    _Float16* xlh   = h16;
-    _Float16* xrh   = x1h;
+    _Float16* e1p = (_Float16*)R;
+    _Float16* e2p = e1p + (size_t)E * 64;
+    _Float16* Yb    = (_Float16*)R;
+    _Float16* skiph = Yb + (size_t)N * 256;
+    _Float16* qtp   = skiph + (size_t)N * 256;
+    _Float16* xaccb = qtp + (size_t)N * 128;
+    _Float16* wab   = xaccb + (size_t)N * 256;
+    float*    lb    = (float*)(wab + (size_t)N * 128);
+    _Float16* e4p = (_Float16*)R;
+    _Float16* xlh = h16;
+    _Float16* xrh = x1h;
     size_t base_off = off;
     _Float16* eap = (_Float16*)alloc((size_t)E * 32 * 2);
     int use_eap = (off <= ws_size) ? 1 : 0;
 
     if (base_off > ws_size) return;
 
-    k_prep<<<256, 256, 0, stream>>>(x, N * 64, wq, wk, wv, wskip, wl, wr,
+    k_prep<<<512, 256, 0, stream>>>(x, N * 64, wq, wk, wv, wskip, wl, wr,
                                     w1a, w1b, w2a, w2b, we3, bq, we1, we2, we4,
-                                    xh, Wtq, Wtk, Wtv, Wts, Wtl, Wtr,
+                                    xh, Wts, Gt, Wtl, Wtr,
                                     Wt1a, Wt1b, Wt2a, Wt2b, Mt, cst,
-                                    we3r, Wt1e, Wt2e, Wt4e);
+                                    Wt1e, Wt2e, Wt4e, zt, Bt3);
 
     k_detect<<<1, 256, 0, stream>>>((const unsigned int*)eidx, flag);
     hipMemsetAsync(counts, 0, (size_t)N * 4, stream);
@@ -807,15 +810,17 @@
     const int* dstI = econv + E;
 
     k_scan<<<1, 1024, 0, stream>>>(counts, offs, cursor, N);
-    k_scatter<<<(E + 255) / 256, 256, 0, stream>>>(dstI, srcI, cursor, perm, sperm,
-                                                   pos, E);
-
-    if (use_eap) {
-        k_eap<<<E / 64, 256, 0, stream>>>(ea, pos, eap);
+    if (use_eap)
+        k_scatter<1><<<(E + 255) / 256, 256, 0, stream>>>(dstI, srcI, cursor, perm,
+                                                          sperm, ea, eap, E);
+    else
+        k_scatter<0><<<(E + 255) / 256, 256, 0, stream>>>(dstI, srcI, cursor, perm,
+                                                          sperm, ea, eap, E);
+
+    if (use_eap)
         k_emm<<<E / 64, 256, 0, stream>>>(eap, Wt1e, be1, e1p, Wt2e, be2, e2p, 1);
-    } else {
+    else
         k_egv<<<E / 32, 256, 0, stream>>>(ea, perm, we1, be1, e1p, we2, be2, e2p, 1);
-    }
 
     k_gine2<<<N / 4, 256, 0, stream>>>(xh, e1p, eps1, offs, sperm, h16);
     k_mlp<64><<<N / 64, 256, 0, stream>>>(h16, Wt1a, b1a, Wt1b, b1b, x1h);
@@ -823,18 +828,17 @@
     k_gine2<<<N / 4, 256, 0, stream>>>(x1h, e2p, eps2, offs, sperm, h16);
     k_mlp<32><<<N / 64, 256, 0, stream>>>(h16, Wt2a, b2a, Wt2b, b2b, x2h);
 
-    k_gemm4m<<<dim3(N / 64, 17), 256, 0, stream>>>(x2h,
-                                                   Wtq, bq, Wtk, bk, Wtv, bv,
-                                                   Wts, bskip, Mt, cst,
-                                                   qbh, kbh, vbh, skipb, qtp);
+    k_gemm4m<<<dim3(N / 64, 9), 256, 0, stream>>>(x2h, Gt, Wts, bskip, Mt, cst,
+                                                  Yb, skiph, qtp);
     if (use_eap)
-        k_tconv4<1><<<N / 4, 256, 0, stream>>>(qbh, kbh, vbh, qtp, we3r, eap,
-                                               ea, perm, offs, sperm, skipb);
+        k_tconv5<1><<<N / 4, 256, 0, stream>>>(Yb, qtp, zt, x2h, eap, ea, perm,
+                                               offs, sperm, xaccb, wab, lb);
     else
-        k_tconv4<0><<<N / 4, 256, 0, stream>>>(qbh, kbh, vbh, qtp, we3r, eap,
-                                               ea, perm, offs, sperm, skipb);
-
-    k_gatgemm<<<dim3(N / 64, 2), 256, 0, stream>>>(skipb, Wtl, bl, Wtr, br, xlh, xrh);
+        k_tconv5<0><<<N / 4, 256, 0, stream>>>(Yb, qtp, zt, x2h, eap, ea, perm,
+                                               offs, sperm, xaccb, wab, lb);
+    k_tpost<<<N / 64, 256, 0, stream>>>(xaccb, wab, lb, Bt3, bvv, skiph);
+
+    k_gatgemm<<<N / 64, 256, 0, stream>>>(skiph, Wtl, bl, Wtr, br, xlh, xrh);
     if (use_eap)
         k_emm<<<E / 64, 256, 0, stream>>>(eap, Wt4e, (const float*)nullptr, e4p,
                                           (const _Float16*)nullptr,
```

New measurement: 343.9 us. -14.3%, faster.
